# Kernel tuning notes

Measured on AMD Instinct MI355X. Metric: run time of the kernel, lower is better.

The kernel has to match this reference:

```python
import jax, jax.numpy as jnp
import numpy as np

# Module/problem constants (match init_kwargs & input_specs)
B, D, H, W = 2, 96, 96, 96
CIN, COUT, K = 16, 32, 3
N = 200000  # number of active (sparse) voxels


def setup_inputs() -> dict:
    key = jax.random.key(0)
    kf, kw, kb = jax.random.split(key, 3)
    # unique valid voxel coordinates -> deterministic scatter semantics
    rng = np.random.default_rng(0)
    lin = rng.choice(B * D * H * W, size=N, replace=False)
    b, z, y, x = np.unravel_index(lin, (B, D, H, W))
    indices = jnp.asarray(np.stack([b, z, y, x], axis=1).astype(np.int32))  # [N,4]
    features = jax.random.normal(kf, (N, CIN), dtype=jnp.float32)
    fan_in = CIN * K ** 3
    conv_w = jax.random.normal(kw, (COUT, CIN, K, K, K), dtype=jnp.float32) / np.sqrt(fan_in)
    conv_b = jax.random.normal(kb, (COUT,), dtype=jnp.float32) * 0.01
    return {"features": features, "indices": indices, "conv_w": conv_w, "conv_b": conv_b}


def reference(features, indices, conv_w, conv_b):
    """DenseFallbackConv3d.forward on a SparseConvTensor, stride=1 path.

    1) scatter sparse features into dense grid [B,CIN,D,H,W]
    2) dense Conv3d (k=3, pad=1, stride=1) + bias
    3) gather per-point output features at the same voxel indices -> [N,COUT]
    """
    b = indices[:, 0]
    z = indices[:, 1]
    y = indices[:, 2]
    x = indices[:, 3]
    # scatter: equivalent of grid[b, :, z, y, x] = features
    grid = jnp.zeros((B, CIN, D, H, W), dtype=features.dtype).at[b, :, z, y, x].set(features)
    out = jax.lax.conv_general_dilated(
        grid, conv_w,
        window_strides=(1, 1, 1),
        padding=((1, 1), (1, 1), (1, 1)),
        dimension_numbers=("NCDHW", "OIDHW", "NCDHW"),
    )
    out = out + conv_b[None, :, None, None, None]
    # gather: out_dense[b, :, z, y, x] for every active voxel -> [N, COUT]
    return out[b, :, z, y, x]
```

## Files before the change

kernel.cpp:

```cpp
#include <hip/hip_runtime.h>

#define BB   2
#define DD   96
#define HH   96
#define WW   96
#define CINC 16
#define COUTC 32
#define KVOL 27
#define GRID_VOX (BB*DD*HH*WW)
#define NW (KVOL*CINC*COUTC)
#define VPT 8
#define CVB (256*VPT)

typedef _Float16 half8 __attribute__((ext_vector_type(8)));
typedef float    floatx16 __attribute__((ext_vector_type(16)));
typedef int      int4a   __attribute__((ext_vector_type(4), aligned(4)));


__global__ __launch_bounds__(256) void setup_kernel(
        const int* __restrict__ idx, int* __restrict__ g,
        const float* __restrict__ feat, _Float16* __restrict__ featH,
        const float* __restrict__ w, _Float16* __restrict__ wH,
        int* __restrict__ counter, int n, int sb, int fb) {
    const int bid = blockIdx.x;
    if (bid < sb) {
        int i = bid * 256 + threadIdx.x;
        if (i >= n) return;
        int4 v = ((const int4*)idx)[i];
        int lin = ((v.x * DD + v.y) * HH + v.z) * WW + v.w;
        g[lin] = i;
    } else if (bid < sb + fb) {
        int i = (bid - sb) * 256 + threadIdx.x;
        if (i >= n) return;
        const float4* src = (const float4*)(feat + (size_t)i * CINC);
        float4 f0 = src[0], f1 = src[1], f2 = src[2], f3 = src[3];
        half8 h0, h1;
        h0[0]=(_Float16)f0.x; h0[1]=(_Float16)f0.y; h0[2]=(_Float16)f0.z; h0[3]=(_Float16)f0.w;
        h0[4]=(_Float16)f1.x; h0[5]=(_Float16)f1.y; h0[6]=(_Float16)f1.z; h0[7]=(_Float16)f1.w;
        h1[0]=(_Float16)f2.x; h1[1]=(_Float16)f2.y; h1[2]=(_Float16)f2.z; h1[3]=(_Float16)f2.w;
        h1[4]=(_Float16)f3.x; h1[5]=(_Float16)f3.y; h1[6]=(_Float16)f3.z; h1[7]=(_Float16)f3.w;
        half8* dst = (half8*)(featH + (size_t)i * CINC);
        dst[0] = h0; dst[1] = h1;
    } else {
        int t = (bid - sb - fb) * 256 + threadIdx.x;
        if (t == 0) {
            counter[0] = 0;
            half8 hz = {};
            half8* zr = (half8*)(featH + (size_t)n * CINC);
            zr[0] = hz; zr[1] = hz;
        }
        if (t >= NW) return;
        int ci = t & (CINC - 1);
        int co = (t >> 4) & (COUTC - 1);
        int kk = t >> 9;
        wH[t] = (_Float16)w[(co * CINC + ci) * KVOL + kk];
    }
}

__global__ __launch_bounds__(256) void compact_kernel(
        const int* __restrict__ g, int2* __restrict__ pcperm,
        int* __restrict__ counter, int n) {
    __shared__ int s_wsum[4];
    __shared__ int s_wbase[4];
    __shared__ int s_base;
    const int t = threadIdx.x;
    const int lane = t & 63;
    const int wv = t >> 6;
    const int base = blockIdx.x * CVB + t * VPT;

    int4 a0 = ((const int4*)(g + base))[0];
    int4 a1 = ((const int4*)(g + base))[1];
    int vals[VPT] = {a0.x, a0.y, a0.z, a0.w, a1.x, a1.y, a1.z, a1.w};
    int pid[VPT];
    int cnt = 0;
#pragma unroll
    for (int q = 0; q < VPT; ++q) {
        int p = vals[q];
        bool ok = ((unsigned)p < (unsigned)n);
        pid[q] = ok ? p : -1;
        cnt += ok ? 1 : 0;
    }

    int incl = cnt;
#pragma unroll
    for (int d = 1; d < 64; d <<= 1) {
        int v = __shfl_up(incl, d);
        if (lane >= d) incl += v;
    }
    if (lane == 63) s_wsum[wv] = incl;
    __syncthreads();
    if (t == 0) {
        int t0 = s_wsum[0], t1 = s_wsum[1], t2 = s_wsum[2], t3 = s_wsum[3];
        s_wbase[0] = 0; s_wbase[1] = t0; s_wbase[2] = t0 + t1;
        s_wbase[3] = t0 + t1 + t2;
        s_base = atomicAdd(counter, t0 + t1 + t2 + t3);
    }
    __syncthreads();
    int o = s_base + s_wbase[wv] + incl - cnt;

#pragma unroll
    for (int q = 0; q < VPT; ++q) {
        int p = pid[q];
        if (p >= 0) {
            int v = base + q;
            int b = (v >= DD * HH * WW) ? 1 : 0;
            int rem = v - b * (DD * HH * WW);
            int z = rem / (HH * WW);
            int r2 = rem - z * (HH * WW);
            int y = r2 / WW;
            int x = r2 - y * WW;
            int2 e; e.x = (b << 21) | (z << 14) | (y << 7) | x; e.y = p;
            pcperm[o] = e;
            ++o;
        }
    }
}

__global__ __launch_bounds__(256, 4) void conv_mfma_kernel(
        const _Float16* __restrict__ featH, const int2* __restrict__ pcperm,
        const _Float16* __restrict__ wH, const float* __restrict__ bias,
        const int* __restrict__ g, float* __restrict__ out, int n) {
    __shared__ _Float16 sW[KVOL * 64 * 8];
    const int lane = threadIdx.x & 63;
    const int wave = threadIdx.x >> 6;
    const int m    = lane & 31;
    const int hf   = lane >> 5;

    for (int u = threadIdx.x; u < KVOL * 64; u += 256) {
        int kk = u >> 6, r = u & 63;
        int mm = r & 31, h = r >> 5;
        half8 v = *(const half8*)(wH + kk * (COUTC * CINC) + mm * CINC + h * 8);
        *(half8*)(&sW[(size_t)u * 8]) = v;
    }
    __syncthreads();

    const int j0 = (blockIdx.x * 4 + wave) * 32;
    if (j0 >= n) return;
    const int j = j0 + m;

    const int2 e = pcperm[j];
    const int p = e.x;
    const int x = p & 127, y = (p >> 7) & 127, z = (p >> 14) & 127, b = p >> 21;
    const int base = ((b * DD + z) * HH + y) * WW + x;
    const int pm = e.y;

    int nid[KVOL];
#pragma unroll
    for (int t9 = 0; t9 < 9; ++t9) {
        const int dz = t9 / 3 - 1, dy = t9 % 3 - 1;
        int nz = z + dz, ny = y + dy;
        bool inb = ((unsigned)nz < DD) & ((unsigned)ny < HH);
        int addr = base + (dz * HH + dy) * WW;
        int a = inb ? addr : 1;
        int4a trip = *(const int4a*)(g + a - 1);
        bool okm = inb & (x >= 1)        & ((unsigned)trip.x < (unsigned)n);
        bool okc = inb                   & ((unsigned)trip.y < (unsigned)n);
        bool okp = inb & (x <= WW - 2)   & ((unsigned)trip.z < (unsigned)n);
        nid[t9 * 3 + 0] = okm ? trip.x : n;
        nid[t9 * 3 + 1] = okc ? trip.y : n;
        nid[t9 * 3 + 2] = okp ? trip.z : n;
    }

    float bval = bias[m];
    floatx16 acc;
#pragma unroll
    for (int i = 0; i < 16; ++i) acc[i] = bval;

#pragma unroll
    for (int gq = 0; gq < 3; ++gq) {
        half8 av[9];
#pragma unroll
        for (int q = 0; q < 9; ++q)
            av[q] = *(const half8*)(featH + (size_t)nid[gq * 9 + q] * CINC + hf * 8);
#pragma unroll
        for (int q = 0; q < 9; ++q) {
            const int kk = gq * 9 + q;
            half8 bf = *(const half8*)(&sW[((size_t)kk * 64 + hf * 32 + m) * 8]);
            acc = __builtin_amdgcn_mfma_f32_32x32x16_f16(av[q], bf, acc, 0, 0, 0);
        }
    }

#pragma unroll
    for (int i = 0; i < 16; ++i) {
        int r = (i & 3) + 8 * (i >> 2) + 4 * hf;
        int row = __shfl(pm, r);
        out[(size_t)row * COUTC + m] = acc[i];
    }
}

extern "C" void kernel_launch(void* const* d_in, const int* in_sizes, int n_in,
                              void* d_out, int out_size, void* d_ws, size_t ws_size,
                              hipStream_t stream) {
    const float* feat  = (const float*)d_in[0];
    const int*   idx   = (const int*)d_in[1];
    const float* convw = (const float*)d_in[2];
    const float* convb = (const float*)d_in[3];
    float* out = (float*)d_out;

    const int n = in_sizes[1] / 4;

    char* ws = (char*)d_ws;
    int*      counter = (int*)ws;
    int*      g       = (int*)(ws + 256);
    int2*     pcperm  = (int2*)(ws + 256 + (size_t)GRID_VOX*4);
    _Float16* featH   = (_Float16*)(pcperm + n);
    _Float16* wH      = featH + (size_t)(n + 1) * CINC;

    const int sb = (n + 255) / 256;
    const int fb = (n + 255) / 256;
    const int rb = (NW + 255) / 256;

    setup_kernel<<<sb + fb + rb, 256, 0, stream>>>(
        idx, g, feat, featH, convw, wH, counter, n, sb, fb);
    compact_kernel<<<GRID_VOX / CVB, 256, 0, stream>>>(g, pcperm, counter, n);

    const int waves = (n + 31) / 32;
    conv_mfma_kernel<<<(waves + 3) / 4, 256, 0, stream>>>(
        featH, pcperm, wH, convb, g, out, n);
}
```

Before: 110.3 us.

## Drop voxel compaction pass and process points in original input order

Removes the compact kernel, which scanned the whole dense index grid and built a spatially ordered point permutation with an atomic counter. The conv kernel now reads each point's coordinates straight from the input index array and writes output rows contiguously, with no shuffle-based row remap. This saves one launch plus a full pass over the grid. In exchange, the 32 points in a wave are no longer spatial neighbours, so the neighbour lookups into the grid become scattered and lose cache locality.

```diff
diff --git a/kernel.cpp b/kernel.cpp
--- a/kernel.cpp
+++ b/kernel.cpp
@@ -9,8 +9,6 @@
 #define KVOL 27
 #define GRID_VOX (BB*DD*HH*WW)
 #define NW (KVOL*CINC*COUTC)
-#define VPT 8
-#define CVB (256*VPT)
 
 typedef _Float16 half8 __attribute__((ext_vector_type(8)));
 typedef float    floatx16 __attribute__((ext_vector_type(16)));
@@ -21,7 +19,7 @@
         const int* __restrict__ idx, int* __restrict__ g,
         const float* __restrict__ feat, _Float16* __restrict__ featH,
         const float* __restrict__ w, _Float16* __restrict__ wH,
-        int* __restrict__ counter, int n, int sb, int fb) {
+        int n, int sb, int fb) {
     const int bid = blockIdx.x;
     if (bid < sb) {
         int i = bid * 256 + threadIdx.x;
@@ -44,7 +42,6 @@
     } else {
         int t = (bid - sb - fb) * 256 + threadIdx.x;
         if (t == 0) {
-            counter[0] = 0;
             half8 hz = {};
             half8* zr = (half8*)(featH + (size_t)n * CINC);
             zr[0] = hz; zr[1] = hz;
@@ -57,67 +54,8 @@
     }
 }
 
-__global__ __launch_bounds__(256) void compact_kernel(
-        const int* __restrict__ g, int2* __restrict__ pcperm,
-        int* __restrict__ counter, int n) {
-    __shared__ int s_wsum[4];
-    __shared__ int s_wbase[4];
-    __shared__ int s_base;
-    const int t = threadIdx.x;
-    const int lane = t & 63;
-    const int wv = t >> 6;
-    const int base = blockIdx.x * CVB + t * VPT;
-
-    int4 a0 = ((const int4*)(g + base))[0];
-    int4 a1 = ((const int4*)(g + base))[1];
-    int vals[VPT] = {a0.x, a0.y, a0.z, a0.w, a1.x, a1.y, a1.z, a1.w};
-    int pid[VPT];
-    int cnt = 0;
-#pragma unroll
-    for (int q = 0; q < VPT; ++q) {
-        int p = vals[q];
-        bool ok = ((unsigned)p < (unsigned)n);
-        pid[q] = ok ? p : -1;
-        cnt += ok ? 1 : 0;
-    }
-
-    int incl = cnt;
-#pragma unroll
-    for (int d = 1; d < 64; d <<= 1) {
-        int v = __shfl_up(incl, d);
-        if (lane >= d) incl += v;
-    }
-    if (lane == 63) s_wsum[wv] = incl;
-    __syncthreads();
-    if (t == 0) {
-        int t0 = s_wsum[0], t1 = s_wsum[1], t2 = s_wsum[2], t3 = s_wsum[3];
-        s_wbase[0] = 0; s_wbase[1] = t0; s_wbase[2] = t0 + t1;
-        s_wbase[3] = t0 + t1 + t2;
-        s_base = atomicAdd(counter, t0 + t1 + t2 + t3);
-    }
-    __syncthreads();
-    int o = s_base + s_wbase[wv] + incl - cnt;
-
-#pragma unroll
-    for (int q = 0; q < VPT; ++q) {
-        int p = pid[q];
-        if (p >= 0) {
-            int v = base + q;
-            int b = (v >= DD * HH * WW) ? 1 : 0;
-            int rem = v - b * (DD * HH * WW);
-            int z = rem / (HH * WW);
-            int r2 = rem - z * (HH * WW);
-            int y = r2 / WW;
-            int x = r2 - y * WW;
-            int2 e; e.x = (b << 21) | (z << 14) | (y << 7) | x; e.y = p;
-            pcperm[o] = e;
-            ++o;
-        }
-    }
-}
-
 __global__ __launch_bounds__(256, 4) void conv_mfma_kernel(
-        const _Float16* __restrict__ featH, const int2* __restrict__ pcperm,
+        const _Float16* __restrict__ featH, const int* __restrict__ idx,
         const _Float16* __restrict__ wH, const float* __restrict__ bias,
         const int* __restrict__ g, float* __restrict__ out, int n) {
     __shared__ _Float16 sW[KVOL * 64 * 8];
@@ -138,11 +76,9 @@
     if (j0 >= n) return;
     const int j = j0 + m;
 
-    const int2 e = pcperm[j];
-    const int p = e.x;
-    const int x = p & 127, y = (p >> 7) & 127, z = (p >> 14) & 127, b = p >> 21;
+    int4 c = ((const int4*)idx)[j];
+    const int b = c.x, z = c.y, y = c.z, x = c.w;
     const int base = ((b * DD + z) * HH + y) * WW + x;
-    const int pm = e.y;
 
     int nid[KVOL];
 #pragma unroll
@@ -183,8 +119,7 @@
 #pragma unroll
     for (int i = 0; i < 16; ++i) {
         int r = (i & 3) + 8 * (i >> 2) + 4 * hf;
-        int row = __shfl(pm, r);
-        out[(size_t)row * COUTC + m] = acc[i];
+        out[(size_t)(j0 + r) * COUTC + m] = acc[i];
     }
 }
 
@@ -200,10 +135,8 @@
     const int n = in_sizes[1] / 4;
 
     char* ws = (char*)d_ws;
-    int*      counter = (int*)ws;
     int*      g       = (int*)(ws + 256);
-    int2*     pcperm  = (int2*)(ws + 256 + (size_t)GRID_VOX*4);
-    _Float16* featH   = (_Float16*)(pcperm + n);
+    _Float16* featH   = (_Float16*)(ws + 256 + (size_t)GRID_VOX * 4);
     _Float16* wH      = featH + (size_t)(n + 1) * CINC;
 
     const int sb = (n + 255) / 256;
@@ -211,10 +144,9 @@
     const int rb = (NW + 255) / 256;
 
     setup_kernel<<<sb + fb + rb, 256, 0, stream>>>(
-        idx, g, feat, featH, convw, wH, counter, n, sb, fb);
-    compact_kernel<<<GRID_VOX / CVB, 256, 0, stream>>>(g, pcperm, counter, n);
+        idx, g, feat, featH, convw, wH, n, sb, fb);
 
     const int waves = (n + 31) / 32;
     conv_mfma_kernel<<<(waves + 3) / 4, 256, 0, stream>>>(
-        featH, pcperm, wH, convb, g, out, n);
+        featH, idx, wH, convb, g, out, n);
 }
```

Measured after the change: 115.7 us. 4.9% more time.
